# Performance work log

Hardware: AMD Instinct MI355X
Metric: run time of the kernel (lower is better)

Reference implementation:

```python
import jax, jax.numpy as jnp
import numpy as np
from jax import lax

MAX_LEN = 40
SOS_ID = 2
VOCAB, EMB, HID, CTX = 32000, 512, 1024, 64
H2 = HID // 2
B, S = 256, 128


def gru_cell(x, h, wih, whh, bih, bhh):
    # PyTorch GRU equations: gates ordered (r, z, n)
    gx = x @ wih.T + bih
    gh = h @ whh.T + bhh
    rx, zx, nx = jnp.split(gx, 3, axis=-1)
    rh, zh, nh = jnp.split(gh, 3, axis=-1)
    r = jax.nn.sigmoid(rx + rh)
    z = jax.nn.sigmoid(zx + zh)
    n = jnp.tanh(nx + r * nh)
    return (1.0 - z) * n + z * h


def setup_inputs() -> dict:
    key = jax.random.key(0)
    ks = jax.random.split(key, 16)
    sd = 0.02
    emb_table = jax.random.normal(ks[0], (VOCAB, EMB), jnp.float32) * sd
    emb_table = emb_table.at[0].set(0.0)  # padding_idx=0
    def w(k, shape):
        return jax.random.normal(k, shape, jnp.float32) * sd
    inp = {
        "input_ids": jax.random.randint(ks[1], (B, S), 0, VOCAB),
        "context_vec": jax.random.normal(ks[2], (B, CTX), jnp.float32),
        "emb_table": emb_table,
        # encoder fwd direction
        "enc_wih_f": w(ks[3], (3 * H2, EMB)),
        "enc_whh_f": w(ks[4], (3 * H2, H2)),
        "enc_bih_f": w(ks[5], (3 * H2,)),
        "enc_bhh_f": w(ks[6], (3 * H2,)),
        # encoder bwd direction
        "enc_wih_b": w(ks[7], (3 * H2, EMB)),
        "enc_whh_b": w(ks[8], (3 * H2, H2)),
        "enc_bih_b": w(ks[9], (3 * H2,)),
        "enc_bhh_b": w(ks[10], (3 * H2,)),
        # decoder GRU: input = emb + hidden + context
        "dec_wih": w(ks[11], (3 * HID, EMB + HID + CTX)),
        "dec_whh": w(ks[12], (3 * HID, HID)),
        "dec_bih": w(ks[13], (3 * HID,)),
        "dec_bhh": w(ks[14], (3 * HID,)),
        "wout": w(ks[15], (VOCAB, HID)),
        "bout": jnp.zeros((VOCAB,), jnp.float32),
    }
    return inp


def reference(input_ids, context_vec, emb_table,
              enc_wih_f, enc_whh_f, enc_bih_f, enc_bhh_f,
              enc_wih_b, enc_whh_b, enc_bih_b, enc_bhh_b,
              dec_wih, dec_whh, dec_bih, dec_bhh, wout, bout):
    b = input_ids.shape[0]
    emb = emb_table[input_ids]                      # [B,S,E]
    emb_t = jnp.swapaxes(emb, 0, 1)                 # [S,B,E]

    def enc_f(h, x):
        return gru_cell(x, h, enc_wih_f, enc_whh_f, enc_bih_f, enc_bhh_f), None

    def enc_b(h, x):
        return gru_cell(x, h, enc_wih_b, enc_whh_b, enc_bih_b, enc_bhh_b), None

    h0 = jnp.zeros((b, H2), emb.dtype)
    hf, _ = lax.scan(enc_f, h0, emb_t)
    hb, _ = lax.scan(enc_b, h0, emb_t[::-1])
    # replicate torch's h_n.view(batch, -1) on a (2,B,H2) tensor (contiguous reshape)
    encoder_ctx = jnp.stack([hf, hb], axis=0).reshape(b, HID)   # [B,HID]

    ctx = jnp.concatenate([encoder_ctx, context_vec], axis=-1)  # [B,HID+CTX]
    h_dec0 = jnp.zeros((b, HID), emb.dtype)
    prev0 = jnp.full((b,), SOS_ID, dtype=jnp.int32)

    def dec_step(carry, _):
        h, prev = carry
        x = jnp.concatenate([emb_table[prev], ctx], axis=-1)
        h = gru_cell(x, h, dec_wih, dec_whh, dec_bih, dec_bhh)
        logits = h @ wout.T + bout                  # [B,V]
        probs = jax.nn.softmax(logits, axis=-1)
        nxt = jnp.argmax(probs, axis=-1).astype(jnp.int32)
        sel = jnp.take_along_axis(probs, nxt[:, None], axis=1)[:, 0]
        lp = jnp.log(sel + 1e-12)
        return (h, nxt), (nxt, lp)

    (_, _), (toks, lps) = lax.scan(dec_step, (h_dec0, prev0), None, length=MAX_LEN)
    return toks.T, lps.T   # [B,MAX_LEN] tokens, [B,MAX_LEN] log-probs
```

## Files before the change

### kernel.cpp

```cpp
#include <hip/hip_runtime.h>
#include <hip/hip_bf16.h>
#include <math.h>

#define B_    256
#define S_    128
#define EMB_  512
#define H2_   512
#define HID_  1024
#define CTX_  64
#define VOC_  32000
#define TMAX_ 40
#define SOS_  2

typedef unsigned short u16;
typedef __attribute__((ext_vector_type(8))) short short8;
typedef __attribute__((ext_vector_type(4))) float f32x4;

__device__ __forceinline__ float4 ld4(const float* p) {
    return *reinterpret_cast<const float4*>(p);
}
__device__ __forceinline__ float sigmoidf_(float x) { return 1.f / (1.f + expf(-x)); }
__device__ __forceinline__ u16 f2bf(float x) {
    union { float f; unsigned int u; } v; v.f = x;
    unsigned int r = v.u + 0x7FFFu + ((v.u >> 16) & 1u);
    return (u16)(r >> 16);
}
__device__ __forceinline__ unsigned pk2(float a, float b) {
    float2 t; t.x = a; t.y = b;
    __hip_bfloat162 h = __float22bfloat162_rn(t);
    return *reinterpret_cast<unsigned*>(&h);
}
__device__ __forceinline__ void merge_top2(float& v1, int& i1, float& v2, int& i2,
                                           float ov1, int oi1, float ov2, int oi2)
{
    if (ov1 > v1 || (ov1 == v1 && oi1 < i1)) {
        float tv = v1; int ti = i1;
        v1 = ov1; i1 = oi1;
        if (ov2 > tv || (ov2 == tv && oi2 < ti)) { v2 = ov2; i2 = oi2; }
        else                                     { v2 = tv;  i2 = ti;  }
    } else {
        if (ov1 > v2 || (ov1 == v2 && oi1 < i2)) { v2 = ov1; i2 = oi1; }
    }
}

template<int BM, int BN, int TM, int TN, int AMODE, int BGATHER, int BIASM>
__launch_bounds__(256)
__global__ void gemm_nt(const float* __restrict__ Ap,
                        const int*   __restrict__ ids,
                        const float* __restrict__ Ex,
                        const float* __restrict__ Bp, int ldb, int bofs,
                        const float* __restrict__ bias,
                        const float* __restrict__ addsrc,
                        float* __restrict__ Cp, int ldc,
                        int lda, int K, int s_base, int sdir)
{
    constexpr int BK = 32;
    __shared__ float As[BK][BM + 4];
    __shared__ float Bs[BK][BN + 4];
    const int t  = threadIdx.x;
    const int tx = t & 15, ty = t >> 4;
    const int m_base = blockIdx.y * BM;
    const int n_base = blockIdx.x * BN;

    float acc[TM][TN];
#pragma unroll
    for (int i = 0; i < TM; ++i)
#pragma unroll
        for (int j = 0; j < TN; ++j) acc[i][j] = 0.f;

    constexpr int A_PER = BM * BK / 4 / 256;
    constexpr int B_PER = BN * BK / 4 / 256;

    for (int k0 = 0; k0 < K; k0 += BK) {
#pragma unroll
        for (int j = 0; j < A_PER; ++j) {
            int f   = t + j * 256;
            int row = f >> 3;
            int kk  = (f & 7) << 2;
            int m   = m_base + row;
            float4 v;
            if constexpr (AMODE == 0) {
                v = ld4(Ap + (size_t)m * lda + k0 + kk);
            } else if constexpr (AMODE == 3) {
                int id = ids[m];
                v = ld4(Ex + (size_t)id * EMB_ + k0 + kk);
            } else {
                int k = k0 + kk;
                if (k < HID_) v = ld4(Ap + (size_t)m * HID_ + k);
                else          v = ld4(Ex + (size_t)m * CTX_ + (k - HID_));
            }
            As[kk + 0][row] = v.x; As[kk + 1][row] = v.y;
            As[kk + 2][row] = v.z; As[kk + 3][row] = v.w;
        }
#pragma unroll
        for (int j = 0; j < B_PER; ++j) {
            int f   = t + j * 256;
            int row = f >> 3;
            int kk  = (f & 7) << 2;
            float4 v;
            if constexpr (BGATHER == 1) {
                int n = n_base + row;
                int s = n >> 8, b = n & 255;
                int id = ids[b * S_ + s_base + sdir * s];
                v = ld4(Ex + (size_t)id * EMB_ + k0 + kk);
            } else {
                v = ld4(Bp + (size_t)(n_base + row) * ldb + bofs + k0 + kk);
            }
            Bs[kk + 0][row] = v.x; Bs[kk + 1][row] = v.y;
            Bs[kk + 2][row] = v.z; Bs[kk + 3][row] = v.w;
        }
        __syncthreads();
#pragma unroll
        for (int kk = 0; kk < BK; ++kk) {
            float a[TM], b[TN];
            *(float4*)&a[0] = ld4(&As[kk][ty * TM]);
            if constexpr (TM == 8) *(float4*)&a[4] = ld4(&As[kk][ty * TM + 4]);
            *(float4*)&b[0] = ld4(&Bs[kk][tx * TN]);
            if constexpr (TN == 8) *(float4*)&b[4] = ld4(&Bs[kk][tx * TN + 4]);
#pragma unroll
            for (int i = 0; i < TM; ++i)
#pragma unroll
                for (int j = 0; j < TN; ++j) acc[i][j] += a[i] * b[j];
        }
        __syncthreads();
    }
#pragma unroll
    for (int i = 0; i < TM; ++i) {
        int m = m_base + ty * TM + i;
#pragma unroll
        for (int j = 0; j < TN; ++j) {
            int n = n_base + tx * TN + j;
            float v = acc[i][j];
            if (bias) v += BIASM ? bias[m] : bias[n];
            if (addsrc) v += addsrc[(size_t)m * ldc + n];
            Cp[(size_t)m * ldc + n] = v;
        }
    }
}

__global__ void whh_trans(const float* __restrict__ whh_f, const float* __restrict__ whh_b,
                          float* __restrict__ whhU_f, float* __restrict__ whhU_b)
{
    int idx = blockIdx.x * 256 + threadIdx.x;
    const float* src = blockIdx.y ? whh_b : whh_f;
    float*       dst = blockIdx.y ? whhU_b : whhU_f;
    int k  = idx / 1536;
    int rem = idx - k * 1536;
    int g  = rem >> 9;
    int u  = rem & 511;
    dst[idx] = src[(size_t)(g * 512 + u) * 512 + k];
}

__global__ void wbf_conv(const float* __restrict__ wout, unsigned* __restrict__ wbf)
{
    int idx = blockIdx.x * 256 + threadIdx.x;
    float2 v = *reinterpret_cast<const float2*>(wout + (size_t)idx * 2);
    wbf[idx] = pk2(v.x, v.y);
}

union EncSM {
    struct { float hbuf[2][512][4]; } rec;
    struct { float As[32][132]; float Bs[32][132]; } gx;
};

__launch_bounds__(512)
__global__ void enc_fused(const float* __restrict__ grec_f, const float* __restrict__ grec_b,
                          float* __restrict__ gout_f, float* __restrict__ gout_b,
                          const float* __restrict__ whhU_f, const float* __restrict__ whhU_b,
                          const float* __restrict__ bhh_f, const float* __restrict__ bhh_b,
                          const float* __restrict__ wih_f, const float* __restrict__ wih_b,
                          const float* __restrict__ bih_f, const float* __restrict__ bih_b,
                          const int* __restrict__ ids, const float* __restrict__ emb,
                          float* __restrict__ hT, int do_rec, int gx_chunk, int nsteps)
{
    __shared__ __align__(16) EncSM sm;
    const int t = threadIdx.x;
    const int idx = blockIdx.x;
    const int grp = idx & 15;

    if (grp >= 8) {
        if (gx_chunk < 0) return;
        const int g = (idx >> 4) * 8 + (grp - 8);
        const int dz  = g >= 192;
        const int t192 = dz ? g - 192 : g;
        const int m_base = (t192 & 15) * 128;
        const int n_base = (t192 >> 4) * 128;
        const float* W    = dz ? wih_b : wih_f;
        const float* bias = dz ? bih_b : bih_f;
        float*       Cp   = dz ? gout_b : gout_f;
        const int s_base  = dz ? (127 - 8 * gx_chunk) : (8 * gx_chunk);
        const int sdir    = dz ? -1 : 1;
        const int tx = t & 31, ty = t >> 5;

        float acc[8][4];
#pragma unroll
        for (int i = 0; i < 8; ++i)
#pragma unroll
            for (int j = 0; j < 4; ++j) acc[i][j] = 0.f;

        for (int k0 = 0; k0 < 512; k0 += 32) {
#pragma unroll
            for (int j = 0; j < 2; ++j) {
                int f   = t + j * 512;
                int row = f >> 3;
                int kk  = (f & 7) << 2;
                int m   = m_base + row;
                int s   = m >> 8, b = m & 255;
                int id  = ids[b * S_ + s_base + sdir * s];
                float4 v = ld4(emb + (size_t)id * EMB_ + k0 + kk);
                sm.gx.As[kk + 0][row] = v.x; sm.gx.As[kk + 1][row] = v.y;
                sm.gx.As[kk + 2][row] = v.z; sm.gx.As[kk + 3][row] = v.w;
                float4 wv = ld4(W + (size_t)(n_base + row) * 512 + k0 + kk);
                sm.gx.Bs[kk + 0][row] = wv.x; sm.gx.Bs[kk + 1][row] = wv.y;
                sm.gx.Bs[kk + 2][row] = wv.z; sm.gx.Bs[kk + 3][row] = wv.w;
            }
            __syncthreads();
#pragma unroll
            for (int kk = 0; kk < 32; ++kk) {
                float a[8], b[4];
                *(float4*)&a[0] = ld4(&sm.gx.As[kk][ty * 8]);
                *(float4*)&a[4] = ld4(&sm.gx.As[kk][ty * 8 + 4]);
                *(float4*)&b[0] = ld4(&sm.gx.Bs[kk][tx * 4]);
#pragma unroll
                for (int i = 0; i < 8; ++i)
#pragma unroll
                    for (int j = 0; j < 4; ++j) acc[i][j] += a[i] * b[j];
            }
            __syncthreads();
        }
#pragma unroll
        for (int i = 0; i < 8; ++i) {
            int m = m_base + ty * 8 + i;
#pragma unroll
            for (int j = 0; j < 4; ++j) {
                int n = n_base + tx * 4 + j;
                Cp[(size_t)m * 1536 + n] = acc[i][j] + bias[n];
            }
        }
        return;
    }

    if (idx >= 256 || !do_rec) return;
    const int xcd = idx & 7;
    const int dir = xcd >> 2;
    const int local = (idx >> 4) * 4 + (xcd & 3);
    const int r0 = local * 4;
    const float* gx  = dir ? grec_b : grec_f;
    const float* whx = dir ? whhU_b : whhU_f;
    const float* bhh = dir ? bhh_b : bhh_f;
    float* hTd = hT + (size_t)dir * (256 * 512);

    const int u = t;

#pragma unroll
    for (int r = 0; r < 4; ++r)
        sm.rec.hbuf[0][u][r] = hTd[(size_t)(r0 + r) * 512 + u];
    const float bh0 = bhh[u], bh1 = bhh[512 + u], bh2 = bhh[1024 + u];
    __syncthreads();

    for (int st = 0; st < nsteps; ++st) {
        const int cur = st & 1, nxt = cur ^ 1;

        float gx0[4], gx1[4], gx2[4];
#pragma unroll
        for (int r = 0; r < 4; ++r) {
            size_t base = (size_t)((st << 8) + r0 + r) * 1536 + u;
            gx0[r] = gx[base];
            gx1[r] = gx[base + 512];
            gx2[r] = gx[base + 1024];
        }

        float acc0[4] = {0.f,0.f,0.f,0.f};
        float acc1[4] = {0.f,0.f,0.f,0.f};
        float acc2[4] = {0.f,0.f,0.f,0.f};
        const float* wp = whx + u;
#pragma unroll 8
        for (int kk = 0; kk < 512; ++kk) {
            float4 hv = *(const float4*)&sm.rec.hbuf[cur][kk][0];
            float w0 = wp[0], w1 = wp[512], w2 = wp[1024];
            const float* hvp = (const float*)&hv;
#pragma unroll
            for (int r = 0; r < 4; ++r) {
                acc0[r] += w0 * hvp[r];
                acc1[r] += w1 * hvp[r];
                acc2[r] += w2 * hvp[r];
            }
            wp += 1536;
        }

#pragma unroll
        for (int r = 0; r < 4; ++r) {
            float hold = sm.rec.hbuf[cur][u][r];
            float rg = sigmoidf_(gx0[r] + acc0[r] + bh0);
            float zg = sigmoidf_(gx1[r] + acc1[r] + bh1);
            float ng = tanhf(gx2[r] + rg * (acc2[r] + bh2));
            sm.rec.hbuf[nxt][u][r] = (1.f - zg) * ng + zg * hold;
        }
        __syncthreads();
    }

    const int lb = nsteps & 1;
#pragma unroll
    for (int r = 0; r < 4; ++r)
        hTd[(size_t)(r0 + r) * 512 + u] = sm.rec.hbuf[lb][u][r];
}

__global__ void zerof(float* __restrict__ p, int n)
{
    int i = blockIdx.x * 256 + threadIdx.x;
    if (i < n) p[i] = 0.f;
}

__global__ void init_dec(float* __restrict__ hdec, u16* __restrict__ hbf, int* __restrict__ prev)
{
    int i = blockIdx.x * 256 + threadIdx.x;
    hdec[i] = 0.f; hbf[i] = 0;
    if (i < B_) prev[i] = SOS_;
}

__global__ void hcat_build(const float* __restrict__ hT, float* __restrict__ hcat)
{
    int idx = blockIdx.x * 256 + threadIdx.x;
    int b = idx >> 10, k = idx & 1023;
    int d = b >> 7;
    int rr = ((2 * b) & 255) + (k >> 9);
    int kk = k & 511;
    hcat[idx] = hT[(size_t)d * 131072 + (size_t)rr * 512 + kk];
}

__launch_bounds__(256)
__global__ void dec_gemm2(const float* __restrict__ hdec, const int* __restrict__ prev,
                          const float* __restrict__ emb,
                          const float* __restrict__ dwhh, const float* __restrict__ dwih,
                          const float* __restrict__ dbhh, const float* __restrict__ gctx,
                          float* __restrict__ ghbuf, float* __restrict__ gibuf)
{
    constexpr int BK = 32;
    __shared__ float As[BK][68];
    __shared__ float Bs[BK][68];
    const int t  = threadIdx.x;
    const int tx = t & 15, ty = t >> 4;
    const bool isH = blockIdx.y < 4;
    const int m_base = (isH ? blockIdx.y : (blockIdx.y - 4)) * 64;
    const int n_base = blockIdx.x * 64;
    const int K   = isH ? 1024 : 512;
    const float* Bp = isH ? dwhh : dwih;
    const int ldb  = isH ? 1024 : 1600;
    float* Cp = isH ? ghbuf : gibuf;

    float acc[4][4];
#pragma unroll
    for (int i = 0; i < 4; ++i)
#pragma unroll
        for (int j = 0; j < 4; ++j) acc[i][j] = 0.f;

    for (int k0 = 0; k0 < K; k0 += BK) {
#pragma unroll
        for (int j = 0; j < 2; ++j) {
            int f   = t + j * 256;
            int row = f >> 3;
            int kk  = (f & 7) << 2;
            int m   = m_base + row;
            float4 v;
            if (isH) v = ld4(hdec + (size_t)m * HID_ + k0 + kk);
            else     v = ld4(emb + (size_t)prev[m] * EMB_ + k0 + kk);
            As[kk + 0][row] = v.x; As[kk + 1][row] = v.y;
            As[kk + 2][row] = v.z; As[kk + 3][row] = v.w;
            float4 w = ld4(Bp + (size_t)(n_base + row) * ldb + k0 + kk);
            Bs[kk + 0][row] = w.x; Bs[kk + 1][row] = w.y;
            Bs[kk + 2][row] = w.z; Bs[kk + 3][row] = w.w;
        }
        __syncthreads();
#pragma unroll
        for (int kk = 0; kk < BK; ++kk) {
            float a[4], b[4];
            *(float4*)&a[0] = ld4(&As[kk][ty * 4]);
            *(float4*)&b[0] = ld4(&Bs[kk][tx * 4]);
#pragma unroll
            for (int i = 0; i < 4; ++i)
#pragma unroll
                for (int j = 0; j < 4; ++j) acc[i][j] += a[i] * b[j];
        }
        __syncthreads();
    }
#pragma unroll
    for (int i = 0; i < 4; ++i) {
        int m = m_base + ty * 4 + i;
#pragma unroll
        for (int j = 0; j < 4; ++j) {
            int n = n_base + tx * 4 + j;
            float v = acc[i][j];
            if (isH) v += dbhh[n];
            else     v += gctx[(size_t)m * 3072 + n];
            Cp[(size_t)m * 3072 + n] = v;
        }
    }
}

__global__ void dec_combine(const float* __restrict__ gi, const float* __restrict__ gh,
                            float* __restrict__ hdec, u16* __restrict__ hbf)
{
    int idx = blockIdx.x * 256 + threadIdx.x;
    int b = idx >> 10, u = idx & 1023;
    size_t gb = (size_t)b * 3072;
    float r = sigmoidf_(gi[gb + u]            + gh[gb + u]);
    float z = sigmoidf_(gi[gb + HID_ + u]     + gh[gb + HID_ + u]);
    float n = tanhf    (gi[gb + 2 * HID_ + u] + r * gh[gb + 2 * HID_ + u]);
    float v = (1.f - z) * n + z * hdec[idx];
    hdec[idx] = v;
    hbf[idx] = f2bf(v);
}

__launch_bounds__(512)
__global__ void gemm_logits(const u16* __restrict__ A, const float* __restrict__ Wf,
                            const u16* __restrict__ Wbf,
                            const float* __restrict__ bias,
                            float* __restrict__ pmax, float* __restrict__ psum,
                            float* __restrict__ ptv, int* __restrict__ pti)
{
    __shared__ u16 As[256][72];
    __shared__ u16 Bs[128][72];
    const int t = threadIdx.x;
    const int lane = t & 63, wave = t >> 6;
    const int wm = (wave & 3) * 64, wn = (wave >> 2) * 64;
    const int n0 = blockIdx.x * 128;
    f32x4 acc[4][4];
#pragma unroll
    for (int i = 0; i < 4; ++i)
#pragma unroll
        for (int j = 0; j < 4; ++j) acc[i][j] = (f32x4){0.f, 0.f, 0.f, 0.f};
    const int arow = t >> 1, aoff = (t & 1) * 32;
    const int brow = t >> 2, boff = (t & 3) * 16;

    for (int k0 = 0; k0 < 1024; k0 += 64) {
#pragma unroll
        for (int q = 0; q < 4; ++q) {
            *(uint4*)&As[arow][aoff + q * 8] =
                *(const uint4*)(A + (size_t)arow * 1024 + k0 + aoff + q * 8);
        }
        if (Wbf) {
            const u16* wr = Wbf + (size_t)(n0 + brow) * 1024 + k0 + boff;
            *(uint4*)&Bs[brow][boff]     = *(const uint4*)(wr);
            *(uint4*)&Bs[brow][boff + 8] = *(const uint4*)(wr + 8);
        } else {
            const float* wr = Wf + (size_t)(n0 + brow) * 1024 + k0 + boff;
#pragma unroll
            for (int q = 0; q < 2; ++q) {
                float4 x = ld4(wr + q * 8);
                float4 y = ld4(wr + q * 8 + 4);
                uint4 o;
                o.x = pk2(x.x, x.y); o.y = pk2(x.z, x.w);
                o.z = pk2(y.x, y.y); o.w = pk2(y.z, y.w);
                *(uint4*)&Bs[brow][boff + q * 8] = o;
            }
        }
        __syncthreads();
#pragma unroll
        for (int s = 0; s < 2; ++s) {
            short8 a[4], b[4];
            int j0 = s * 32 + (lane >> 4) * 8;
#pragma unroll
            for (int i = 0; i < 4; ++i) {
                a[i] = *(const short8*)&As[wm + i * 16 + (lane & 15)][j0];
                b[i] = *(const short8*)&Bs[wn + i * 16 + (lane & 15)][j0];
            }
#pragma unroll
            for (int i = 0; i < 4; ++i)
#pragma unroll
                for (int j = 0; j < 4; ++j)
                    acc[i][j] = __builtin_amdgcn_mfma_f32_16x16x32_bf16(a[i], b[j], acc[i][j], 0, 0, 0);
        }
        __syncthreads();
    }

    const int htile = blockIdx.x * 2 + (wn >> 6);
    float bn[4]; int jx[4];
#pragma unroll
    for (int j = 0; j < 4; ++j) { jx[j] = n0 + wn + j * 16 + (lane & 15); bn[j] = bias[jx[j]]; }
#pragma unroll
    for (int i = 0; i < 4; ++i) {
#pragma unroll
        for (int rr = 0; rr < 4; ++rr) {
            float v[4];
#pragma unroll
            for (int j = 0; j < 4; ++j) v[j] = acc[i][j][rr] + bn[j];
            float v1 = v[0], v2 = -3.4e38f; int i1 = jx[0], i2 = 0x7fffffff;
#pragma unroll
            for (int j = 1; j < 4; ++j) {
                if (v[j] > v1)      { v2 = v1; i2 = i1; v1 = v[j]; i1 = jx[j]; }
                else if (v[j] > v2) { v2 = v[j]; i2 = jx[j]; }
            }
#pragma unroll
            for (int mask = 1; mask <= 8; mask <<= 1) {
                float ov1 = __shfl_xor(v1, mask), ov2 = __shfl_xor(v2, mask);
                int   oi1 = __shfl_xor(i1, mask), oi2 = __shfl_xor(i2, mask);
                merge_top2(v1, i1, v2, i2, ov1, oi1, ov2, oi2);
            }
            float rmax = v1;
            float s = 0.f;
#pragma unroll
            for (int j = 0; j < 4; ++j) s += expf(v[j] - rmax);
#pragma unroll
            for (int mask = 1; mask <= 8; mask <<= 1) s += __shfl_xor(s, mask);
            if ((lane & 15) == 0) {
                int row = wm + i * 16 + (lane >> 4) * 4 + rr;
                size_t base = (size_t)row * 500 + htile;
                pmax[base] = rmax; psum[base] = s;
                ptv[base * 2] = v1; ptv[base * 2 + 1] = v2;
                pti[base * 2] = i1; pti[base * 2 + 1] = i2;
            }
        }
    }
}

__launch_bounds__(256)
__global__ void dec_reduce(const float* __restrict__ pmax, const float* __restrict__ psum,
                           const float* __restrict__ ptv, const int* __restrict__ pti,
                           const float* __restrict__ hdec, const float* __restrict__ wout,
                           const float* __restrict__ bout,
                           float* __restrict__ out, int* __restrict__ prev, int tstep)
{
    __shared__ float sv[256]; __shared__ int sti[256]; __shared__ int ssl[256];
    __shared__ float cvv[1000]; __shared__ int cii[1000];
    __shared__ float c8v[8]; __shared__ int c8i[8]; __shared__ float c8e[8];
    const int b = blockIdx.x, tid = threadIdx.x;
    const float* pm = pmax + (size_t)b * 500;
    const float* ps = psum + (size_t)b * 500;

    float m = -3.4e38f;
    for (int i = tid; i < 500; i += 256) m = fmaxf(m, pm[i]);
    sv[tid] = m; __syncthreads();
    for (int off = 128; off; off >>= 1) { if (tid < off) sv[tid] = fmaxf(sv[tid], sv[tid + off]); __syncthreads(); }
    float gmax = sv[0]; __syncthreads();

    float s = 0.f;
    for (int i = tid; i < 500; i += 256) s += ps[i] * expf(pm[i] - gmax);
    sv[tid] = s; __syncthreads();
    for (int off = 128; off; off >>= 1) { if (tid < off) sv[tid] += sv[tid + off]; __syncthreads(); }
    float gsum = sv[0]; __syncthreads();

    for (int i = tid; i < 1000; i += 256) { cvv[i] = ptv[(size_t)b * 1000 + i]; cii[i] = pti[(size_t)b * 1000 + i]; }
    __syncthreads();

    for (int c = 0; c < 8; ++c) {
        float bv = -3.4e38f; int bi = 0x7fffffff, bs = 0;
        for (int i = tid; i < 1000; i += 256) {
            float v = cvv[i]; int ix = cii[i];
            if (v > bv || (v == bv && ix < bi)) { bv = v; bi = ix; bs = i; }
        }
        sv[tid] = bv; sti[tid] = bi; ssl[tid] = bs; __syncthreads();
        for (int off = 128; off; off >>= 1) {
            if (tid < off) {
                if (sv[tid + off] > sv[tid] ||
                    (sv[tid + off] == sv[tid] && sti[tid + off] < sti[tid])) {
                    sv[tid] = sv[tid + off]; sti[tid] = sti[tid + off]; ssl[tid] = ssl[tid + off];
                }
            }
            __syncthreads();
        }
        if (tid == 0) { c8v[c] = sv[0]; c8i[c] = sti[0]; cvv[ssl[0]] = -3.4e38f; }
        __syncthreads();
    }

    {
        int lane = tid & 63, wv = tid >> 6;
        const float* hr = hdec + (size_t)b * HID_;
        for (int c = wv; c < 8; c += 4) {
            const float* wr = wout + (size_t)c8i[c] * HID_;
            float a = 0.f;
            for (int k = lane * 4; k < HID_; k += 256) {
                float4 x = ld4(hr + k), y = ld4(wr + k);
                a += x.x * y.x + x.y * y.y + x.z * y.z + x.w * y.w;
            }
#pragma unroll
            for (int off = 32; off; off >>= 1) a += __shfl_down(a, off);
            if (lane == 0) c8e[c] = a + bout[c8i[c]];
        }
    }
    __syncthreads();

    if (tid == 0) {
        float bv = c8e[0]; int bi = c8i[0]; float av = c8v[0];
        for (int c = 1; c < 8; ++c)
            if (c8e[c] > bv || (c8e[c] == bv && c8i[c] < bi)) { bv = c8e[c]; bi = c8i[c]; av = c8v[c]; }
        float p = expf(av - gmax) / gsum;
        float lp = logf(p + 1e-12f);
        out[(size_t)b * TMAX_ + tstep] = (float)bi;
        out[B_ * TMAX_ + (size_t)b * TMAX_ + tstep] = lp;
        prev[b] = bi;
    }
}

extern "C" void kernel_launch(void* const* d_in, const int* in_sizes, int n_in,
                              void* d_out, int out_size, void* d_ws, size_t ws_size,
                              hipStream_t stream)
{
    const int*   ids   = (const int*)  d_in[0];
    const float* cvec  = (const float*)d_in[1];
    const float* emb   = (const float*)d_in[2];
    const float* wih_f = (const float*)d_in[3];
    const float* whh_f = (const float*)d_in[4];
    const float* bih_f = (const float*)d_in[5];
    const float* bhh_f = (const float*)d_in[6];
    const float* wih_b = (const float*)d_in[7];
    const float* whh_b = (const float*)d_in[8];
    const float* bih_b = (const float*)d_in[9];
    const float* bhh_b = (const float*)d_in[10];
    const float* dwih  = (const float*)d_in[11];
    const float* dwhh  = (const float*)d_in[12];
    const float* dbih  = (const float*)d_in[13];
    const float* dbhh  = (const float*)d_in[14];
    const float* wout  = (const float*)d_in[15];
    const float* bout  = (const float*)d_in[16];
    float* out = (float*)d_out;

    float* w      = (float*)d_ws;
    float* buf0_f = w;
    float* buf0_b = w + 3145728;
    float* buf1_f = w + 6291456;
    float* buf1_b = w + 9437184;
    float* hT     = w + 12582912;
    float* hcat   = w + 12845056;
    float* hdec   = w + 13107200;
    float* gctx   = w + 13369344;
    u16*   hdecb  = (u16*)(w + 14155776);
    int*   prev   = (int*)(w + 14286848);
    float* whhU_f = w + 14287104;
    float* whhU_b = w + 15073536;
    u16*   wbf    = (u16*)(w + 15859968);
    const int use_wbf = (ws_size >= (size_t)(15859968 + 16384000) * 4);
    float* gibuf  = buf0_f;
    float* ghbuf  = buf0_f + 786432;
    float* pmax   = buf0_f + 1572864;
    float* psum   = buf0_f + 1700864;
    float* ptv    = buf0_f + 1828864;
    int*   pti    = (int*)(buf0_f + 2084864);

    zerof<<<1024, 256, 0, stream>>>(hT, 262144);
    init_dec<<<1024, 256, 0, stream>>>(hdec, hdecb, prev);
    whh_trans<<<dim3(3072, 2), 256, 0, stream>>>(whh_f, whh_b, whhU_f, whhU_b);

    enc_fused<<<768, 512, 0, stream>>>(
        buf0_f, buf0_b, buf0_f, buf0_b, whhU_f, whhU_b, bhh_f, bhh_b,
        wih_f, wih_b, bih_f, bih_b, ids, emb, hT, 0, 0, 8);
    for (int c = 1; c < 16; ++c) {
        float* rf = ((c - 1) & 1) ? buf1_f : buf0_f;
        float* rb = ((c - 1) & 1) ? buf1_b : buf0_b;
        float* of = (c & 1) ? buf1_f : buf0_f;
        float* ob = (c & 1) ? buf1_b : buf0_b;
        enc_fused<<<768, 512, 0, stream>>>(
            rf, rb, of, ob, whhU_f, whhU_b, bhh_f, bhh_b,
            wih_f, wih_b, bih_f, bih_b, ids, emb, hT, 1, c, 8);
    }
    enc_fused<<<768, 512, 0, stream>>>(
        buf1_f, buf1_b, buf1_f, buf1_b, whhU_f, whhU_b, bhh_f, bhh_b,
        wih_f, wih_b, bih_f, bih_b, ids, emb, hT, 1, -1, 8);

    hcat_build<<<1024, 256, 0, stream>>>(hT, hcat);

    if (use_wbf)
        wbf_conv<<<64000, 256, 0, stream>>>(wout, (unsigned*)wbf);

    gemm_nt<64, 64, 4, 4, 2, 0, 0><<<dim3(48, 4), 256, 0, stream>>>(
        hcat, nullptr, cvec, dwih, 1600, 512, dbih, nullptr,
        gctx, 3072, 1024, 1088, 0, 0);

    for (int t = 0; t < TMAX_; ++t) {
        dec_gemm2<<<dim3(48, 8), 256, 0, stream>>>(
            hdec, prev, emb, dwhh, dwih, dbhh, gctx, ghbuf, gibuf);
        dec_combine<<<1024, 256, 0, stream>>>(gibuf, ghbuf, hdec, hdecb);
        gemm_logits<<<dim3(250, 1), 512, 0, stream>>>(
            hdecb, wout, use_wbf ? wbf : (const u16*)nullptr, bout,
            pmax, psum, ptv, pti);
        dec_reduce<<<256, 256, 0, stream>>>(pmax, psum, ptv, pti,
                                            hdec, wout, bout, out, prev, t);
    }
}
```

Baseline: 10.13 ms.

## Overlap decoder hidden-gate GEMM with logits GEMM and repack encoder Whh

The decoder step is restructured so that the h@Whh gate GEMM for the next step runs as extra blocks inside the logits kernel, since it depends only on the new hidden state and not on the argmax token. The emb@Wih part becomes its own smaller kernel that runs after the reduce step. A partial bf16 copy of wout is also built when the workspace is small, and the encoder Whh is repacked so the r and z weights load together as one float2. The aim is fewer serialized launches per step and better use of the GPU while the logits GEMM runs, at the cost of more kernel complexity and shared-memory unions.

```diff
diff --git a/kernel.cpp b/kernel.cpp
--- a/kernel.cpp
+++ b/kernel.cpp
@@ -139,21 +139,30 @@
 }
 
 __global__ void whh_trans(const float* __restrict__ whh_f, const float* __restrict__ whh_b,
-                          float* __restrict__ whhU_f, float* __restrict__ whhU_b)
+                          float* __restrict__ whhA_f, float* __restrict__ whhB_f,
+                          float* __restrict__ whhA_b, float* __restrict__ whhB_b)
 {
     int idx = blockIdx.x * 256 + threadIdx.x;
     const float* src = blockIdx.y ? whh_b : whh_f;
-    float*       dst = blockIdx.y ? whhU_b : whhU_f;
-    int k  = idx / 1536;
-    int rem = idx - k * 1536;
-    int g  = rem >> 9;
-    int u  = rem & 511;
-    dst[idx] = src[(size_t)(g * 512 + u) * 512 + k];
-}
-
-__global__ void wbf_conv(const float* __restrict__ wout, unsigned* __restrict__ wbf)
+    float* dA = blockIdx.y ? whhA_b : whhA_f;
+    float* dB = blockIdx.y ? whhB_b : whhB_f;
+    if (idx < 262144) {
+        int k = idx >> 9, u = idx & 511;
+        float2 v;
+        v.x = src[(size_t)u * 512 + k];
+        v.y = src[(size_t)(512 + u) * 512 + k];
+        *(float2*)&dA[(size_t)idx * 2] = v;
+    } else {
+        int j = idx - 262144;
+        int k = j >> 9, u = j & 511;
+        dB[j] = src[(size_t)(1024 + u) * 512 + k];
+    }
+}
+
+__global__ void wbf_conv(const float* __restrict__ wout, unsigned* __restrict__ wbf, int npairs)
 {
     int idx = blockIdx.x * 256 + threadIdx.x;
+    if (idx >= npairs) return;
     float2 v = *reinterpret_cast<const float2*>(wout + (size_t)idx * 2);
     wbf[idx] = pk2(v.x, v.y);
 }
@@ -166,7 +175,8 @@
 __launch_bounds__(512)
 __global__ void enc_fused(const float* __restrict__ grec_f, const float* __restrict__ grec_b,
                           float* __restrict__ gout_f, float* __restrict__ gout_b,
-                          const float* __restrict__ whhU_f, const float* __restrict__ whhU_b,
+                          const float* __restrict__ whhA_f, const float* __restrict__ whhB_f,
+                          const float* __restrict__ whhA_b, const float* __restrict__ whhB_b,
                           const float* __restrict__ bhh_f, const float* __restrict__ bhh_b,
                           const float* __restrict__ wih_f, const float* __restrict__ wih_b,
                           const float* __restrict__ bih_f, const float* __restrict__ bih_b,
@@ -246,7 +256,8 @@
     const int local = (idx >> 4) * 4 + (xcd & 3);
     const int r0 = local * 4;
     const float* gx  = dir ? grec_b : grec_f;
-    const float* whx = dir ? whhU_b : whhU_f;
+    const float2* wA = (const float2*)(dir ? whhA_b : whhA_f);
+    const float*  wB = dir ? whhB_b : whhB_f;
     const float* bhh = dir ? bhh_b : bhh_f;
     float* hTd = hT + (size_t)dir * (256 * 512);
 
@@ -273,19 +284,21 @@
         float acc0[4] = {0.f,0.f,0.f,0.f};
         float acc1[4] = {0.f,0.f,0.f,0.f};
         float acc2[4] = {0.f,0.f,0.f,0.f};
-        const float* wp = whx + u;
+        const float2* wpA = wA + u;
+        const float*  wpB = wB + u;
 #pragma unroll 8
         for (int kk = 0; kk < 512; ++kk) {
             float4 hv = *(const float4*)&sm.rec.hbuf[cur][kk][0];
-            float w0 = wp[0], w1 = wp[512], w2 = wp[1024];
+            float2 wrz = wpA[0];
+            float  wn  = wpB[0];
             const float* hvp = (const float*)&hv;
 #pragma unroll
             for (int r = 0; r < 4; ++r) {
-                acc0[r] += w0 * hvp[r];
-                acc1[r] += w1 * hvp[r];
-                acc2[r] += w2 * hvp[r];
-            }
-            wp += 1536;
+                acc0[r] += wrz.x * hvp[r];
+                acc1[r] += wrz.y * hvp[r];
+                acc2[r] += wn    * hvp[r];
+            }
+            wpA += 512; wpB += 512;
         }
 
 #pragma unroll
@@ -397,6 +410,63 @@
     }
 }
 
+__launch_bounds__(256)
+__global__ void dec_gi(const int* __restrict__ prev, const float* __restrict__ emb,
+                       const float* __restrict__ dwih, const float* __restrict__ gctx,
+                       float* __restrict__ gibuf)
+{
+    constexpr int BK = 32;
+    __shared__ float As[BK][68];
+    __shared__ float Bs[BK][68];
+    const int t  = threadIdx.x;
+    const int tx = t & 15, ty = t >> 4;
+    const int m_base = blockIdx.y * 64;
+    const int n_base = blockIdx.x * 64;
+
+    float acc[4][4];
+#pragma unroll
+    for (int i = 0; i < 4; ++i)
+#pragma unroll
+        for (int j = 0; j < 4; ++j) acc[i][j] = 0.f;
+
+    for (int k0 = 0; k0 < 512; k0 += BK) {
+#pragma unroll
+        for (int j = 0; j < 2; ++j) {
+            int f   = t + j * 256;
+            int row = f >> 3;
+            int kk  = (f & 7) << 2;
+            int m   = m_base + row;
+            float4 v = ld4(emb + (size_t)prev[m] * EMB_ + k0 + kk);
+            As[kk + 0][row] = v.x; As[kk + 1][row] = v.y;
+            As[kk + 2][row] = v.z; As[kk + 3][row] = v.w;
+            float4 w = ld4(dwih + (size_t)(n_base + row) * 1600 + k0 + kk);
+            Bs[kk + 0][row] = w.x; Bs[kk + 1][row] = w.y;
+            Bs[kk + 2][row] = w.z; Bs[kk + 3][row] = w.w;
+        }
+        __syncthreads();
+#pragma unroll
+        for (int kk = 0; kk < BK; ++kk) {
+            float a[4], b[4];
+            *(float4*)&a[0] = ld4(&As[kk][ty * 4]);
+            *(float4*)&b[0] = ld4(&Bs[kk][tx * 4]);
+#pragma unroll
+            for (int i = 0; i < 4; ++i)
+#pragma unroll
+                for (int j = 0; j < 4; ++j) acc[i][j] += a[i] * b[j];
+        }
+        __syncthreads();
+    }
+#pragma unroll
+    for (int i = 0; i < 4; ++i) {
+        int m = m_base + ty * 4 + i;
+#pragma unroll
+        for (int j = 0; j < 4; ++j) {
+            int n = n_base + tx * 4 + j;
+            gibuf[(size_t)m * 3072 + n] = acc[i][j] + gctx[(size_t)m * 3072 + n];
+        }
+    }
+}
+
 __global__ void dec_combine(const float* __restrict__ gi, const float* __restrict__ gh,
                             float* __restrict__ hdec, u16* __restrict__ hbf)
 {
@@ -411,16 +481,74 @@
     hbf[idx] = f2bf(v);
 }
 
+union DecSM {
+    struct { u16 As[256][72]; u16 Bs[128][72]; } lg;
+    struct { float As[32][68]; float Bs[32][68]; } gh;
+};
+
 __launch_bounds__(512)
-__global__ void gemm_logits(const u16* __restrict__ A, const float* __restrict__ Wf,
-                            const u16* __restrict__ Wbf,
-                            const float* __restrict__ bias,
-                            float* __restrict__ pmax, float* __restrict__ psum,
-                            float* __restrict__ ptv, int* __restrict__ pti)
-{
-    __shared__ u16 As[256][72];
-    __shared__ u16 Bs[128][72];
+__global__ void dec_lh(const u16* __restrict__ A, const float* __restrict__ Wf,
+                       const u16* __restrict__ Wbf, int wbfRows,
+                       const float* __restrict__ bias,
+                       float* __restrict__ pmax, float* __restrict__ psum,
+                       float* __restrict__ ptv, int* __restrict__ pti,
+                       const float* __restrict__ hdec, const float* __restrict__ dwhh,
+                       const float* __restrict__ dbhh, float* __restrict__ ghbuf,
+                       int doGh)
+{
+    __shared__ __align__(16) DecSM sm;
     const int t = threadIdx.x;
+
+    if (blockIdx.y == 1) {
+        if (!doGh || blockIdx.x >= 192) return;
+        const int g  = blockIdx.x;
+        const int m0 = (g / 48) * 64;
+        const int n0 = (g % 48) * 64;
+        const int tx = t & 15, ty = t >> 4;
+
+        float acc[2][4];
+#pragma unroll
+        for (int i = 0; i < 2; ++i)
+#pragma unroll
+            for (int j = 0; j < 4; ++j) acc[i][j] = 0.f;
+
+        for (int k0 = 0; k0 < 1024; k0 += 32) {
+            {
+                int row = t >> 3;
+                int kk  = (t & 7) << 2;
+                float4 v = ld4(hdec + (size_t)(m0 + row) * HID_ + k0 + kk);
+                sm.gh.As[kk + 0][row] = v.x; sm.gh.As[kk + 1][row] = v.y;
+                sm.gh.As[kk + 2][row] = v.z; sm.gh.As[kk + 3][row] = v.w;
+                float4 w = ld4(dwhh + (size_t)(n0 + row) * 1024 + k0 + kk);
+                sm.gh.Bs[kk + 0][row] = w.x; sm.gh.Bs[kk + 1][row] = w.y;
+                sm.gh.Bs[kk + 2][row] = w.z; sm.gh.Bs[kk + 3][row] = w.w;
+            }
+            __syncthreads();
+#pragma unroll
+            for (int kk = 0; kk < 32; ++kk) {
+                float2 a = *(const float2*)&sm.gh.As[kk][ty * 2];
+                float b[4];
+                *(float4*)&b[0] = ld4(&sm.gh.Bs[kk][tx * 4]);
+#pragma unroll
+                for (int j = 0; j < 4; ++j) {
+                    acc[0][j] += a.x * b[j];
+                    acc[1][j] += a.y * b[j];
+                }
+            }
+            __syncthreads();
+        }
+#pragma unroll
+        for (int i = 0; i < 2; ++i) {
+            int m = m0 + ty * 2 + i;
+#pragma unroll
+            for (int j = 0; j < 4; ++j) {
+                int n = n0 + tx * 4 + j;
+                ghbuf[(size_t)m * 3072 + n] = acc[i][j] + dbhh[n];
+            }
+        }
+        return;
+    }
+
     const int lane = t & 63, wave = t >> 6;
     const int wm = (wave & 3) * 64, wn = (wave >> 2) * 64;
     const int n0 = blockIdx.x * 128;
@@ -431,17 +559,18 @@
         for (int j = 0; j < 4; ++j) acc[i][j] = (f32x4){0.f, 0.f, 0.f, 0.f};
     const int arow = t >> 1, aoff = (t & 1) * 32;
     const int brow = t >> 2, boff = (t & 3) * 16;
+    const bool useBf = (n0 + brow) < wbfRows;
 
     for (int k0 = 0; k0 < 1024; k0 += 64) {
 #pragma unroll
         for (int q = 0; q < 4; ++q) {
-            *(uint4*)&As[arow][aoff + q * 8] =
+            *(uint4*)&sm.lg.As[arow][aoff + q * 8] =
                 *(const uint4*)(A + (size_t)arow * 1024 + k0 + aoff + q * 8);
         }
-        if (Wbf) {
+        if (useBf) {
             const u16* wr = Wbf + (size_t)(n0 + brow) * 1024 + k0 + boff;
-            *(uint4*)&Bs[brow][boff]     = *(const uint4*)(wr);
-            *(uint4*)&Bs[brow][boff + 8] = *(const uint4*)(wr + 8);
+            *(uint4*)&sm.lg.Bs[brow][boff]     = *(const uint4*)(wr);
+            *(uint4*)&sm.lg.Bs[brow][boff + 8] = *(const uint4*)(wr + 8);
         } else {
             const float* wr = Wf + (size_t)(n0 + brow) * 1024 + k0 + boff;
 #pragma unroll
@@ -451,7 +580,7 @@
                 uint4 o;
                 o.x = pk2(x.x, x.y); o.y = pk2(x.z, x.w);
                 o.z = pk2(y.x, y.y); o.w = pk2(y.z, y.w);
-                *(uint4*)&Bs[brow][boff + q * 8] = o;
+                *(uint4*)&sm.lg.Bs[brow][boff + q * 8] = o;
             }
         }
         __syncthreads();
@@ -461,8 +590,8 @@
             int j0 = s * 32 + (lane >> 4) * 8;
 #pragma unroll
             for (int i = 0; i < 4; ++i) {
-                a[i] = *(const short8*)&As[wm + i * 16 + (lane & 15)][j0];
-                b[i] = *(const short8*)&Bs[wn + i * 16 + (lane & 15)][j0];
+                a[i] = *(const short8*)&sm.lg.As[wm + i * 16 + (lane & 15)][j0];
+                b[i] = *(const short8*)&sm.lg.Bs[wn + i * 16 + (lane & 15)][j0];
             }
 #pragma unroll
             for (int i = 0; i < 4; ++i)
@@ -625,54 +754,66 @@
     float* gctx   = w + 13369344;
     u16*   hdecb  = (u16*)(w + 14155776);
     int*   prev   = (int*)(w + 14286848);
-    float* whhU_f = w + 14287104;
-    float* whhU_b = w + 15073536;
-    u16*   wbf    = (u16*)(w + 15859968);
-    const int use_wbf = (ws_size >= (size_t)(15859968 + 16384000) * 4);
-    float* gibuf  = buf0_f;
-    float* ghbuf  = buf0_f + 786432;
-    float* pmax   = buf0_f + 1572864;
-    float* psum   = buf0_f + 1700864;
-    float* ptv    = buf0_f + 1828864;
-    int*   pti    = (int*)(buf0_f + 2084864);
+    float* whhA_f = w + 14287104;
+    float* whhB_f = w + 14811392;
+    float* whhA_b = w + 15073536;
+    float* whhB_b = w + 15597824;
+    u16*   wbf_big = (u16*)(w + 15859968);
+    const int big_ws = (ws_size >= (size_t)(15859968 + 16384000) * 4);
+    float* gibuf  = w;
+    float* ghbuf  = w + 786432;
+    float* pmax   = w + 1572864;
+    float* psum   = w + 1700864;
+    float* ptv    = w + 1828864;
+    int*   pti    = (int*)(w + 2084864);
+    u16*   wbf_part = (u16*)(w + 2340864);
+    const int wbfRows = big_ws ? VOC_ : 20992;
+    u16* wbfPtr = big_ws ? wbf_big : wbf_part;
 
     zerof<<<1024, 256, 0, stream>>>(hT, 262144);
     init_dec<<<1024, 256, 0, stream>>>(hdec, hdecb, prev);
-    whh_trans<<<dim3(3072, 2), 256, 0, stream>>>(whh_f, whh_b, whhU_f, whhU_b);
+    whh_trans<<<dim3(2048, 2), 256, 0, stream>>>(whh_f, whh_b,
+                                                 whhA_f, whhB_f, whhA_b, whhB_b);
 
     enc_fused<<<768, 512, 0, stream>>>(
-        buf0_f, buf0_b, buf0_f, buf0_b, whhU_f, whhU_b, bhh_f, bhh_b,
-        wih_f, wih_b, bih_f, bih_b, ids, emb, hT, 0, 0, 8);
+        buf0_f, buf0_b, buf0_f, buf0_b, whhA_f, whhB_f, whhA_b, whhB_b,
+        bhh_f, bhh_b, wih_f, wih_b, bih_f, bih_b, ids, emb, hT, 0, 0, 8);
     for (int c = 1; c < 16; ++c) {
         float* rf = ((c - 1) & 1) ? buf1_f : buf0_f;
         float* rb = ((c - 1) & 1) ? buf1_b : buf0_b;
         float* of = (c & 1) ? buf1_f : buf0_f;
         float* ob = (c & 1) ? buf1_b : buf0_b;
         enc_fused<<<768, 512, 0, stream>>>(
-            rf, rb, of, ob, whhU_f, whhU_b, bhh_f, bhh_b,
-            wih_f, wih_b, bih_f, bih_b, ids, emb, hT, 1, c, 8);
+            rf, rb, of, ob, whhA_f, whhB_f, whhA_b, whhB_b,
+            bhh_f, bhh_b, wih_f, wih_b, bih_f, bih_b, ids, emb, hT, 1, c, 8);
     }
     enc_fused<<<768, 512, 0, stream>>>(
-        buf1_f, buf1_b, buf1_f, buf1_b, whhU_f, whhU_b, bhh_f, bhh_b,
-        wih_f, wih_b, bih_f, bih_b, ids, emb, hT, 1, -1, 8);
+        buf1_f, buf1_b, buf1_f, buf1_b, whhA_f, whhB_f, whhA_b, whhB_b,
+        bhh_f, bhh_b, wih_f, wih_b, bih_f, bih_b, ids, emb, hT, 1, -1, 8);
 
     hcat_build<<<1024, 256, 0, stream>>>(hT, hcat);
 
-    if (use_wbf)
-        wbf_conv<<<64000, 256, 0, stream>>>(wout, (unsigned*)wbf);
+    {
+        int npairs = wbfRows * 512;
+        wbf_conv<<<(npairs + 255) / 256, 256, 0, stream>>>(wout, (unsigned*)wbfPtr, npairs);
+    }
 
     gemm_nt<64, 64, 4, 4, 2, 0, 0><<<dim3(48, 4), 256, 0, stream>>>(
         hcat, nullptr, cvec, dwih, 1600, 512, dbih, nullptr,
         gctx, 3072, 1024, 1088, 0, 0);
 
+    dec_gemm2<<<dim3(48, 8), 256, 0, stream>>>(
+        hdec, prev, emb, dwhh, dwih, dbhh, gctx, ghbuf, gibuf);
+    dec_combine<<<1024, 256, 0, stream>>>(gibuf, ghbuf, hdec, hdecb);
     for (int t = 0; t < TMAX_; ++t) {
-        dec_gemm2<<<dim3(48, 8), 256, 0, stream>>>(
-            hdec, prev, emb, dwhh, dwih, dbhh, gctx, ghbuf, gibuf);
-        dec_combine<<<1024, 256, 0, stream>>>(gibuf, ghbuf, hdec, hdecb);
-        gemm_logits<<<dim3(250, 1), 512, 0, stream>>>(
-            hdecb, wout, use_wbf ? wbf : (const u16*)nullptr, bout,
-            pmax, psum, ptv, pti);
+        dec_lh<<<dim3(250, 2), 512, 0, stream>>>(
+            hdecb, wout, wbfPtr, wbfRows, bout,
+            pmax, psum, ptv, pti, hdec, dwhh, dbhh, ghbuf, (t < TMAX_ - 1));
         dec_reduce<<<256, 256, 0, stream>>>(pmax, psum, ptv, pti,
                                             hdec, wout, bout, out, prev, t);
-    }
-}
+        if (t < TMAX_ - 1) {
+            dec_gi<<<dim3(48, 4), 256, 0, stream>>>(prev, emb, dwih, gctx, gibuf);
+            dec_combine<<<1024, 256, 0, stream>>>(gibuf, ghbuf, hdec, hdecb);
+        }
+    }
+}
```

Result: slower. 12.60 ms (+24.4%).
